# Optimization experiments

Measured on AMD Instinct MI355X. Metric: run time of the kernel, lower is better.

## Reference

```python
import jax, jax.numpy as jnp
import numpy as np

NUM_NODES = 10000
NUM_EDGES = 640000
D_IN = 128
D_OUT = 128


def setup_inputs() -> dict:
    key = jax.random.key(0)
    k1, k2, k3 = jax.random.split(key, 3)
    x = jax.random.normal(k1, (NUM_NODES, D_IN), dtype=jnp.float32)
    edge_index = jax.random.randint(k2, (2, NUM_EDGES), 0, NUM_NODES, dtype=jnp.int32)
    W = jax.random.normal(k3, (D_IN, D_OUT), dtype=jnp.float32) / np.sqrt(D_IN)
    bias = jnp.zeros((D_OUT,), dtype=jnp.float32)
    return {"x": x, "edge_index": edge_index, "W": W, "bias": bias}


def reference(x, edge_index, W, bias):
    num_nodes = x.shape[0]
    # add self-loops
    self_loops = jnp.arange(num_nodes, dtype=edge_index.dtype)
    row = jnp.concatenate([edge_index[0], self_loops])
    col = jnp.concatenate([edge_index[1], self_loops])
    # symmetric normalization D^{-1/2} A D^{-1/2} (degree computed over row)
    deg = jax.ops.segment_sum(jnp.ones_like(row, dtype=jnp.float32), row,
                              num_segments=num_nodes)
    deg_inv_sqrt = jnp.power(deg, -0.5)
    deg_inv_sqrt = jnp.where(jnp.isinf(deg_inv_sqrt), 0.0, deg_inv_sqrt)
    edge_weight = deg_inv_sqrt[row] * deg_inv_sqrt[col]  # [E+N]
    # linear projection (no bias)
    h = x @ W  # [N, D_OUT]
    # gather -> scale -> scatter-sum
    messages = h[row] * edge_weight[:, None]  # [E+N, D_OUT]
    out = jax.ops.segment_sum(messages, col, num_segments=num_nodes)
    return out + bias
```

## Files before the change

### kernel.cpp

```cpp
#include <hip/hip_runtime.h>


#define NNODES 10000
#define NB 64
#define HBLOCK 1024
#define STAGE_CAP 256
#define GROWS 128
#define XPAD 132

__device__ inline unsigned short f2bf(float f) {
    union { float f; unsigned u; } v; v.f = f;
    unsigned r = v.u + 0x7FFFu + ((v.u >> 16) & 1u);
    return (unsigned short)(r >> 16);
}
__device__ inline float bf2f_lo(unsigned u) {
    union { unsigned u; float f; } v; v.u = u << 16; return v.f;
}
__device__ inline float bf2f_hi(unsigned u) {
    union { unsigned u; float f; } v; v.u = u & 0xFFFF0000u; return v.f;
}

__global__ __launch_bounds__(HBLOCK) void histsort_gemm_kernel(
    const int* __restrict__ row, const int* __restrict__ col,
    const float* __restrict__ x, const float* __restrict__ W,
    unsigned* __restrict__ meta, int* __restrict__ outdeg,
    unsigned short* __restrict__ blkcsr, unsigned short* __restrict__ g,
    int N, int E, int EPB) {
    __shared__ __align__(16) char smem[GROWS * XPAD * 4];
    int* hmem = (int*)smem;
    unsigned short* loff16 = (unsigned short*)(smem + 40000);
    int* wsum = (int*)(smem + 60000);
    float* xs = (float*)smem;
    const int tid = threadIdx.x;

    if (blockIdx.x < NB) {
        const int b = blockIdx.x;
        for (int j = tid; j < NNODES; j += HBLOCK) hmem[j] = 0;
        __syncthreads();
        const int e0 = b * EPB, e1 = min(E, e0 + EPB);
        const int span = e1 - e0;
        const bool vec4 = ((((size_t)(row + e0)) | ((size_t)(col + e0))) & 15) == 0;
        const int nq = vec4 ? (span >> 2) : 0;
        const int4* __restrict__ r4p = (const int4*)(row + e0);
        const int4* __restrict__ c4p = (const int4*)(col + e0);
        for (int qi = tid; qi < nq; qi += HBLOCK) {
            int4 r4 = r4p[qi], c4 = c4p[qi];
            atomicAdd((unsigned*)&hmem[r4.x], 1u);
            atomicAdd((unsigned*)&hmem[r4.y], 1u);
            atomicAdd((unsigned*)&hmem[r4.z], 1u);
            atomicAdd((unsigned*)&hmem[r4.w], 1u);
            atomicAdd((unsigned*)&hmem[c4.x], 0x10000u);
            atomicAdd((unsigned*)&hmem[c4.y], 0x10000u);
            atomicAdd((unsigned*)&hmem[c4.z], 0x10000u);
            atomicAdd((unsigned*)&hmem[c4.w], 0x10000u);
        }
        for (int e = e0 + nq * 4 + tid; e < e1; e += HBLOCK) {
            atomicAdd((unsigned*)&hmem[row[e]], 1u);
            atomicAdd((unsigned*)&hmem[col[e]], 0x10000u);
        }
        __syncthreads();
        {
            const int lane = tid & 63, wid = tid >> 6;
            const int i0 = tid * 10;
            const int i1 = min(NNODES, i0 + 10);
            int s = 0;
            for (int i = i0; i < i1; ++i) s += (int)(((unsigned)hmem[i]) >> 16);
            int p = s;
#pragma unroll
            for (int d = 1; d < 64; d <<= 1) {
                int y = __shfl_up(p, d);
                if (lane >= d) p += y;
            }
            if (lane == 63) wsum[wid] = p;
            __syncthreads();
            if (tid < 16) {
                int v = wsum[tid];
#pragma unroll
                for (int d = 1; d < 16; d <<= 1) {
                    int y = __shfl_up(v, d);
                    if (tid >= d) v += y;
                }
                wsum[tid] = v;
            }
            __syncthreads();
            int run = (wid ? wsum[wid - 1] : 0) + (p - s);
            for (int i = i0; i < i1; ++i) {
                loff16[i] = (unsigned short)run;
                run += (int)(((unsigned)hmem[i]) >> 16);
            }
        }
        __syncthreads();
        for (int j = tid; j < NNODES; j += HBLOCK) {
            unsigned v = (unsigned)hmem[j];
            unsigned cnt = v >> 16;
            unsigned lo = (unsigned)loff16[j];
            meta[(size_t)b * NNODES + j] = lo | (cnt << 16);
            int od = (int)(v & 0xFFFFu);
            if (od) atomicAdd(&outdeg[j], od);
            hmem[j] = (int)lo;
        }
        __syncthreads();
        unsigned short* __restrict__ bc = blkcsr + (size_t)b * EPB;
        for (int qi = tid; qi < nq; qi += HBLOCK) {
            int4 r4 = r4p[qi], c4 = c4p[qi];
            int s0 = atomicAdd(&hmem[c4.x], 1);
            bc[s0] = (unsigned short)r4.x;
            int s1 = atomicAdd(&hmem[c4.y], 1);
            bc[s1] = (unsigned short)r4.y;
            int s2 = atomicAdd(&hmem[c4.z], 1);
            bc[s2] = (unsigned short)r4.z;
            int s3 = atomicAdd(&hmem[c4.w], 1);
            bc[s3] = (unsigned short)r4.w;
        }
        for (int e = e0 + nq * 4 + tid; e < e1; e += HBLOCK) {
            int slot = atomicAdd(&hmem[col[e]], 1);
            bc[slot] = (unsigned short)row[e];
        }
    } else {
        const int rowBase = (blockIdx.x - NB) * GROWS;
        {
            const float4* __restrict__ x4g = (const float4*)x;
            float4* __restrict__ xs4 = (float4*)xs;
#pragma unroll
            for (int i = 0; i < 4; ++i) {
                int idx = tid + i * HBLOCK;
                int c16 = idx & 31;
                int r = idx >> 5;
                int gr = rowBase + r;
                float4 v = make_float4(0.f, 0.f, 0.f, 0.f);
                if (gr < N) v = x4g[(size_t)gr * 32 + c16];
                xs4[r * 33 + c16] = v;
            }
        }
        __syncthreads();
        const int w = tid >> 6, lane = tid & 63;
        const int aa = w >> 1, bb = w & 1;
        const int rg = aa * 4 + (lane >> 4);
        const int c4 = bb * 16 + (lane & 15);
        const float4* __restrict__ W4 = (const float4*)W;
        const float* __restrict__ xr0 = xs + (rg * 4 + 0) * XPAD;
        const float* __restrict__ xr1 = xs + (rg * 4 + 1) * XPAD;
        const float* __restrict__ xr2 = xs + (rg * 4 + 2) * XPAD;
        const float* __restrict__ xr3 = xs + (rg * 4 + 3) * XPAD;
        float4 acc0 = make_float4(0.f, 0.f, 0.f, 0.f);
        float4 acc1 = make_float4(0.f, 0.f, 0.f, 0.f);
        float4 acc2 = make_float4(0.f, 0.f, 0.f, 0.f);
        float4 acc3 = make_float4(0.f, 0.f, 0.f, 0.f);
#pragma unroll 2
        for (int k0 = 0; k0 < 128; k0 += 4) {
            float4 a0 = *(const float4*)(xr0 + k0);
            float4 a1 = *(const float4*)(xr1 + k0);
            float4 a2 = *(const float4*)(xr2 + k0);
            float4 a3 = *(const float4*)(xr3 + k0);
#pragma unroll
            for (int j = 0; j < 4; ++j) {
                float4 wv = W4[(k0 + j) * 32 + c4];
                float x0 = ((const float*)&a0)[j];
                float x1 = ((const float*)&a1)[j];
                float x2 = ((const float*)&a2)[j];
                float x3 = ((const float*)&a3)[j];
                acc0.x = fmaf(x0, wv.x, acc0.x);
                acc0.y = fmaf(x0, wv.y, acc0.y);
                acc0.z = fmaf(x0, wv.z, acc0.z);
                acc0.w = fmaf(x0, wv.w, acc0.w);
                acc1.x = fmaf(x1, wv.x, acc1.x);
                acc1.y = fmaf(x1, wv.y, acc1.y);
                acc1.z = fmaf(x1, wv.z, acc1.z);
                acc1.w = fmaf(x1, wv.w, acc1.w);
                acc2.x = fmaf(x2, wv.x, acc2.x);
                acc2.y = fmaf(x2, wv.y, acc2.y);
                acc2.z = fmaf(x2, wv.z, acc2.z);
                acc2.w = fmaf(x2, wv.w, acc2.w);
                acc3.x = fmaf(x3, wv.x, acc3.x);
                acc3.y = fmaf(x3, wv.y, acc3.y);
                acc3.z = fmaf(x3, wv.z, acc3.z);
                acc3.w = fmaf(x3, wv.w, acc3.w);
            }
        }
        ushort4* __restrict__ g4 = (ushort4*)g;
        const int r0 = rowBase + rg * 4;
        float4 accs[4] = { acc0, acc1, acc2, acc3 };
#pragma unroll
        for (int i = 0; i < 4; ++i) {
            int gr = r0 + i;
            if (gr < N) {
                ushort4 o;
                o.x = f2bf(accs[i].x);
                o.y = f2bf(accs[i].y);
                o.z = f2bf(accs[i].z);
                o.w = f2bf(accs[i].w);
                g4[(size_t)gr * 32 + c4] = o;
            }
        }
    }
}

__global__ __launch_bounds__(256) void gather_kernel(
    const int* __restrict__ outdeg, const unsigned* __restrict__ meta,
    const unsigned short* __restrict__ blkcsr,
    const unsigned short* __restrict__ g, const float* __restrict__ bias,
    float* __restrict__ out, int N, int EPB) {
    __shared__ unsigned short stage[4][STAGE_CAP];
    __shared__ float dstage[4][STAGE_CAP];
    const int wv = threadIdx.x >> 6;
    const int lane = threadIdx.x & 63;
    const int c = (int)((blockIdx.x * blockDim.x + threadIdx.x) >> 6);
    const bool act = (c < N);

    unsigned m = act ? meta[(size_t)lane * NNODES + c] : 0u;
    int sl = (int)(m & 0xFFFFu);
    int cn = (int)(m >> 16);
    int p = cn;
#pragma unroll
    for (int d = 1; d < 64; d <<= 1) {
        int y = __shfl_up(p, d);
        if (lane >= d) p += y;
    }
    int excl = p - cn;
    int L = __shfl(p, 63);
    if (act && cn) {
        const unsigned short* seg = blkcsr + (size_t)lane * EPB + sl;
        for (int k = 0; k < cn; ++k) {
            int r = (int)seg[k];
            stage[wv][excl + k] = (unsigned short)r;
            dstage[wv][excl + k] = rsqrtf(1.0f + (float)outdeg[r]);
        }
    }
    __syncthreads();
    if (!act) return;

    const int q = lane >> 4;
    const int l16 = lane & 15;
    const uint4* __restrict__ g4 = (const uint4*)g;
    const float dc = rsqrtf(1.0f + (float)outdeg[c]);

    float al0 = 0.f, ah0 = 0.f, al1 = 0.f, ah1 = 0.f;
    float al2 = 0.f, ah2 = 0.f, al3 = 0.f, ah3 = 0.f;

    if (q == 0) {
        uint4 w = g4[(size_t)c * 16 + l16];
        al0 = fmaf(bf2f_lo(w.x), dc, al0); ah0 = fmaf(bf2f_hi(w.x), dc, ah0);
        al1 = fmaf(bf2f_lo(w.y), dc, al1); ah1 = fmaf(bf2f_hi(w.y), dc, ah1);
        al2 = fmaf(bf2f_lo(w.z), dc, al2); ah2 = fmaf(bf2f_hi(w.z), dc, ah2);
        al3 = fmaf(bf2f_lo(w.w), dc, al3); ah3 = fmaf(bf2f_hi(w.w), dc, ah3);
    }

    for (int base = 0; base < L; base += 64) {
        int cnt = min(64, L - base);
#pragma unroll
        for (int t = 0; t < 64; t += 4) {
            int j = t + q;
            if (j < cnt) {
                int r = (int)stage[wv][base + j];
                float ds = dstage[wv][base + j];
                uint4 w = g4[(size_t)r * 16 + l16];
                al0 = fmaf(bf2f_lo(w.x), ds, al0); ah0 = fmaf(bf2f_hi(w.x), ds, ah0);
                al1 = fmaf(bf2f_lo(w.y), ds, al1); ah1 = fmaf(bf2f_hi(w.y), ds, ah1);
                al2 = fmaf(bf2f_lo(w.z), ds, al2); ah2 = fmaf(bf2f_hi(w.z), ds, ah2);
                al3 = fmaf(bf2f_lo(w.w), ds, al3); ah3 = fmaf(bf2f_hi(w.w), ds, ah3);
            }
        }
    }
    al0 += __shfl(al0, lane ^ 32); ah0 += __shfl(ah0, lane ^ 32);
    al1 += __shfl(al1, lane ^ 32); ah1 += __shfl(ah1, lane ^ 32);
    al2 += __shfl(al2, lane ^ 32); ah2 += __shfl(ah2, lane ^ 32);
    al3 += __shfl(al3, lane ^ 32); ah3 += __shfl(ah3, lane ^ 32);
    al0 += __shfl(al0, lane ^ 16); ah0 += __shfl(ah0, lane ^ 16);
    al1 += __shfl(al1, lane ^ 16); ah1 += __shfl(ah1, lane ^ 16);
    al2 += __shfl(al2, lane ^ 16); ah2 += __shfl(ah2, lane ^ 16);
    al3 += __shfl(al3, lane ^ 16); ah3 += __shfl(ah3, lane ^ 16);

    if (lane < 32) {
        int oi = ((lane & 15) << 1) | (lane >> 4);
        float4 bv = ((const float4*)bias)[oi];
        float4 o;
        if (lane < 16) {
            o.x = fmaf(al0, dc, bv.x);
            o.y = fmaf(ah0, dc, bv.y);
            o.z = fmaf(al1, dc, bv.z);
            o.w = fmaf(ah1, dc, bv.w);
        } else {
            o.x = fmaf(al2, dc, bv.x);
            o.y = fmaf(ah2, dc, bv.y);
            o.z = fmaf(al3, dc, bv.z);
            o.w = fmaf(ah3, dc, bv.w);
        }
        ((float4*)out)[(size_t)c * 32 + oi] = o;
    }
}

extern "C" void kernel_launch(void* const* d_in, const int* in_sizes, int n_in,
                              void* d_out, int out_size, void* d_ws, size_t ws_size,
                              hipStream_t stream) {
    const float* x    = (const float*)d_in[0];
    const int*   ei   = (const int*)d_in[1];
    const float* W    = (const float*)d_in[2];
    const float* bias = (const float*)d_in[3];
    float* out = (float*)d_out;

    int N = in_sizes[0] / 128;
    int E = in_sizes[1] / 2;
    const int* row = ei;
    const int* col = ei + E;
    int EPB = (E + NB - 1) / NB;

    auto align256 = [](size_t v) { return (v + 255) & ~(size_t)255; };
    char* p = (char*)d_ws;
    int*            outdeg = (int*)p;            p += align256((size_t)N * 4);
    unsigned*       meta   = (unsigned*)p;       p += align256((size_t)NB * N * 4);
    unsigned short* blkcsr = (unsigned short*)p; p += align256((size_t)NB * EPB * 2);
    unsigned short* g      = (unsigned short*)p; p += align256((size_t)N * 128 * 2);

    hipMemsetAsync(outdeg, 0, (size_t)N * 4, stream);

    int gemmBlocks = (N + GROWS - 1) / GROWS;
    histsort_gemm_kernel<<<NB + gemmBlocks, HBLOCK, 0, stream>>>(
        row, col, x, W, meta, outdeg, blkcsr, g, N, E, EPB);

    int gBlocks = (N + 3) / 4;
    gather_kernel<<<gBlocks, 256, 0, stream>>>(
        outdeg, meta, blkcsr, g, bias, out, N, EPB);
}
```

Baseline: 105.8 us.

## Replace per-block CSR segments with fixed-capacity per-node buckets via global atomics

Each histogram block now reserves space in a per-destination bucket of 256 slots using a global atomicAdd on a per-node count. This replaces the block-local prefix scan and the 64-by-N meta table. The gather kernel reads each node's contiguous bucket directly and broadcasts source indices and degree scales with shuffles, so it no longer needs the strided meta loads, the in-wave scan or the shared-memory staging. In exchange it adds many global atomics in the sort phase and a larger, sparser CSR buffer. Correctness now depends on no node's in-degree exceeding the 256-slot cap.

```diff
diff --git a/kernel.cpp b/kernel.cpp
--- a/kernel.cpp
+++ b/kernel.cpp
@@ -3,8 +3,8 @@
 
 #define NNODES 10000
 #define NB 64
+#define CAP 256
 #define HBLOCK 1024
-#define STAGE_CAP 256
 #define GROWS 128
 #define XPAD 132
 
@@ -23,13 +23,11 @@
 __global__ __launch_bounds__(HBLOCK) void histsort_gemm_kernel(
     const int* __restrict__ row, const int* __restrict__ col,
     const float* __restrict__ x, const float* __restrict__ W,
-    unsigned* __restrict__ meta, int* __restrict__ outdeg,
-    unsigned short* __restrict__ blkcsr, unsigned short* __restrict__ g,
+    int* __restrict__ gcount, int* __restrict__ outdeg,
+    unsigned short* __restrict__ csr, unsigned short* __restrict__ g,
     int N, int E, int EPB) {
     __shared__ __align__(16) char smem[GROWS * XPAD * 4];
     int* hmem = (int*)smem;
-    unsigned short* loff16 = (unsigned short*)(smem + 40000);
-    int* wsum = (int*)(smem + 60000);
     float* xs = (float*)smem;
     const int tid = threadIdx.x;
 
@@ -59,62 +57,30 @@
             atomicAdd((unsigned*)&hmem[col[e]], 0x10000u);
         }
         __syncthreads();
-        {
-            const int lane = tid & 63, wid = tid >> 6;
-            const int i0 = tid * 10;
-            const int i1 = min(NNODES, i0 + 10);
-            int s = 0;
-            for (int i = i0; i < i1; ++i) s += (int)(((unsigned)hmem[i]) >> 16);
-            int p = s;
-#pragma unroll
-            for (int d = 1; d < 64; d <<= 1) {
-                int y = __shfl_up(p, d);
-                if (lane >= d) p += y;
-            }
-            if (lane == 63) wsum[wid] = p;
-            __syncthreads();
-            if (tid < 16) {
-                int v = wsum[tid];
-#pragma unroll
-                for (int d = 1; d < 16; d <<= 1) {
-                    int y = __shfl_up(v, d);
-                    if (tid >= d) v += y;
-                }
-                wsum[tid] = v;
-            }
-            __syncthreads();
-            int run = (wid ? wsum[wid - 1] : 0) + (p - s);
-            for (int i = i0; i < i1; ++i) {
-                loff16[i] = (unsigned short)run;
-                run += (int)(((unsigned)hmem[i]) >> 16);
-            }
-        }
-        __syncthreads();
         for (int j = tid; j < NNODES; j += HBLOCK) {
             unsigned v = (unsigned)hmem[j];
-            unsigned cnt = v >> 16;
-            unsigned lo = (unsigned)loff16[j];
-            meta[(size_t)b * NNODES + j] = lo | (cnt << 16);
             int od = (int)(v & 0xFFFFu);
+            int cnt = (int)(v >> 16);
             if (od) atomicAdd(&outdeg[j], od);
-            hmem[j] = (int)lo;
-        }
-        __syncthreads();
-        unsigned short* __restrict__ bc = blkcsr + (size_t)b * EPB;
+            int base = 0;
+            if (cnt) base = atomicAdd(&gcount[j], cnt);
+            hmem[j] = (j << 8) + base;
+        }
+        __syncthreads();
         for (int qi = tid; qi < nq; qi += HBLOCK) {
             int4 r4 = r4p[qi], c4 = c4p[qi];
             int s0 = atomicAdd(&hmem[c4.x], 1);
-            bc[s0] = (unsigned short)r4.x;
+            csr[s0] = (unsigned short)r4.x;
             int s1 = atomicAdd(&hmem[c4.y], 1);
-            bc[s1] = (unsigned short)r4.y;
+            csr[s1] = (unsigned short)r4.y;
             int s2 = atomicAdd(&hmem[c4.z], 1);
-            bc[s2] = (unsigned short)r4.z;
+            csr[s2] = (unsigned short)r4.z;
             int s3 = atomicAdd(&hmem[c4.w], 1);
-            bc[s3] = (unsigned short)r4.w;
+            csr[s3] = (unsigned short)r4.w;
         }
         for (int e = e0 + nq * 4 + tid; e < e1; e += HBLOCK) {
             int slot = atomicAdd(&hmem[col[e]], 1);
-            bc[slot] = (unsigned short)row[e];
+            csr[slot] = (unsigned short)row[e];
         }
     } else {
         const int rowBase = (blockIdx.x - NB) * GROWS;
@@ -195,40 +161,16 @@
     }
 }
 
-__global__ __launch_bounds__(256) void gather_kernel(
-    const int* __restrict__ outdeg, const unsigned* __restrict__ meta,
-    const unsigned short* __restrict__ blkcsr,
-    const unsigned short* __restrict__ g, const float* __restrict__ bias,
-    float* __restrict__ out, int N, int EPB) {
-    __shared__ unsigned short stage[4][STAGE_CAP];
-    __shared__ float dstage[4][STAGE_CAP];
-    const int wv = threadIdx.x >> 6;
+__global__ void gather_kernel(const int* __restrict__ gcount,
+                              const int* __restrict__ outdeg,
+                              const unsigned short* __restrict__ csr,
+                              const unsigned short* __restrict__ g,
+                              const float* __restrict__ bias,
+                              float* __restrict__ out, int n) {
+    const int wave = (blockIdx.x * blockDim.x + threadIdx.x) >> 6;
     const int lane = threadIdx.x & 63;
-    const int c = (int)((blockIdx.x * blockDim.x + threadIdx.x) >> 6);
-    const bool act = (c < N);
-
-    unsigned m = act ? meta[(size_t)lane * NNODES + c] : 0u;
-    int sl = (int)(m & 0xFFFFu);
-    int cn = (int)(m >> 16);
-    int p = cn;
-#pragma unroll
-    for (int d = 1; d < 64; d <<= 1) {
-        int y = __shfl_up(p, d);
-        if (lane >= d) p += y;
-    }
-    int excl = p - cn;
-    int L = __shfl(p, 63);
-    if (act && cn) {
-        const unsigned short* seg = blkcsr + (size_t)lane * EPB + sl;
-        for (int k = 0; k < cn; ++k) {
-            int r = (int)seg[k];
-            stage[wv][excl + k] = (unsigned short)r;
-            dstage[wv][excl + k] = rsqrtf(1.0f + (float)outdeg[r]);
-        }
-    }
-    __syncthreads();
-    if (!act) return;
-
+    if (wave >= n) return;
+    const int c = wave;
     const int q = lane >> 4;
     const int l16 = lane & 15;
     const uint4* __restrict__ g4 = (const uint4*)g;
@@ -245,14 +187,22 @@
         al3 = fmaf(bf2f_lo(w.w), dc, al3); ah3 = fmaf(bf2f_hi(w.w), dc, ah3);
     }
 
-    for (int base = 0; base < L; base += 64) {
-        int cnt = min(64, L - base);
+    const int start = c << 8;
+    const int end = start + gcount[c];
+    for (int base = start; base < end; base += 64) {
+        int idx = base + lane;
+        int src = 0; float dval = 0.f;
+        if (idx < end) {
+            src = (int)csr[idx];
+            dval = rsqrtf(1.0f + (float)outdeg[src]);
+        }
+        int cnt = min(64, end - base);
 #pragma unroll
         for (int t = 0; t < 64; t += 4) {
             int j = t + q;
+            int r = __shfl(src, j);
+            float ds = __shfl(dval, j);
             if (j < cnt) {
-                int r = (int)stage[wv][base + j];
-                float ds = dstage[wv][base + j];
                 uint4 w = g4[(size_t)r * 16 + l16];
                 al0 = fmaf(bf2f_lo(w.x), ds, al0); ah0 = fmaf(bf2f_hi(w.x), ds, ah0);
                 al1 = fmaf(bf2f_lo(w.y), ds, al1); ah1 = fmaf(bf2f_hi(w.y), ds, ah1);
@@ -307,17 +257,18 @@
     auto align256 = [](size_t v) { return (v + 255) & ~(size_t)255; };
     char* p = (char*)d_ws;
     int*            outdeg = (int*)p;            p += align256((size_t)N * 4);
-    unsigned*       meta   = (unsigned*)p;       p += align256((size_t)NB * N * 4);
-    unsigned short* blkcsr = (unsigned short*)p; p += align256((size_t)NB * EPB * 2);
+    int*            gcount = (int*)p;            p += align256((size_t)N * 4);
+    unsigned short* csr    = (unsigned short*)p; p += align256((size_t)N * CAP * 2);
     unsigned short* g      = (unsigned short*)p; p += align256((size_t)N * 128 * 2);
 
-    hipMemsetAsync(outdeg, 0, (size_t)N * 4, stream);
+    size_t cntBytes = (size_t)((char*)csr - (char*)outdeg);
+    hipMemsetAsync(outdeg, 0, cntBytes, stream);
 
     int gemmBlocks = (N + GROWS - 1) / GROWS;
     histsort_gemm_kernel<<<NB + gemmBlocks, HBLOCK, 0, stream>>>(
-        row, col, x, W, meta, outdeg, blkcsr, g, N, E, EPB);
-
-    int gBlocks = (N + 3) / 4;
-    gather_kernel<<<gBlocks, 256, 0, stream>>>(
-        outdeg, meta, blkcsr, g, bias, out, N, EPB);
-}
+        row, col, x, W, gcount, outdeg, csr, g, N, E, EPB);
+
+    long long gthreads = (long long)N * 64;
+    gather_kernel<<<(int)((gthreads + 255) / 256), 256, 0, stream>>>(
+        gcount, outdeg, csr, g, bias, out, N);
+}
```

After: 101.2 us. 1.04x faster.
